# Optimization experiments

Hardware: AMD Instinct MI355X
Metric: run time of the kernel (lower is better)

## Reference

```python
import itertools
import jax, jax.numpy as jnp
import numpy as np

# ---- static config (mirrors args) ----
BS = 4; NUM_SEM = 24; C = 4 + NUM_SEM
H_SCREEN = 240; W_SCREEN = 320
FOV = 60.0
RES = 5; Z_RES = 5
MAP_SIZE_CM = 4800 // 2            # global_downscaling = 2
MAP_CELLS = MAP_SIZE_CM // RES     # 480
VR = 100                           # vision_range
AGENT_HEIGHT = 1.55 * 100.0        # cm
MAX_H = int(360 / Z_RES)           # 72
MIN_H = int(-40 / Z_RES)           # -8
MAP_PRED_THR = 1.0; EXP_PRED_THR = 1.0; CAT_PRED_THR = 5.0
SHIFT_X = VR * RES // 2            # 250 cm (shift_loc)
XC = (W_SCREEN - 1.0) / 2.0
ZC = (H_SCREEN - 1.0) / 2.0
FOCAL = (W_SCREEN / 2.0) / float(np.tan(np.deg2rad(FOV / 2.0)))
DEG2RAD = float(np.pi / 180.0)
R2D = 57.29577951308232


def splat_feat_nd(init_grid, feat, coords):
    # init_grid [B,F,D0,D1,D2], feat [B,F,N], coords [B,3,N] in [-1,1]
    B, Fc = init_grid.shape[0], init_grid.shape[1]
    dims = init_grid.shape[2:]
    grid_flat = init_grid.reshape(B, Fc, -1)
    pos_all, wts_all = [], []
    for d in range(len(dims)):
        Dd = dims[d]
        pos = coords[:, d, :] * (Dd / 2.0) + Dd / 2.0   # [B,N]
        fl = jnp.floor(pos)
        pd, wd = [], []
        for off in (0.0, 1.0):
            p = fl + off
            safe = ((p > 0) & (p < Dd)).astype(pos.dtype)
            wd.append((1.0 - jnp.abs(pos - p)) * safe)
            pd.append(p * safe)
        pos_all.append(pd); wts_all.append(wd)
    bidx = jnp.arange(B)[:, None, None]
    fidx = jnp.arange(Fc)[None, :, None]
    for corner in itertools.product((0, 1), repeat=len(dims)):
        index = jnp.zeros_like(pos_all[0][0])
        wts = jnp.ones_like(pos_all[0][0])
        for d in range(len(dims)):
            index = index * dims[d] + pos_all[d][corner[d]]
            wts = wts * wts_all[d][corner[d]]
        idx = index.astype(jnp.int32)[:, None, :]        # [B,1,N]
        grid_flat = grid_flat.at[bidx, fidx, idx].add(feat * wts[:, None, :])
    return jnp.round(grid_flat).reshape(init_grid.shape)


def affine_grid(theta, H, W):
    # align_corners=True base grid; theta [B,2,3] -> grid [B,H,W,2]
    xs = jnp.linspace(-1.0, 1.0, W)
    ys = jnp.linspace(-1.0, 1.0, H)
    gx, gy = jnp.meshgrid(xs, ys)                        # [H,W]
    base = jnp.stack([gx, gy, jnp.ones_like(gx)], axis=-1)
    return jnp.einsum('hwk,bjk->bhwj', base, theta)


def grid_sample(img, grid):
    # bilinear, zero padding, align_corners=True. img [B,C,H,W], grid [B,Ho,Wo,2]
    B, Cc, H, W = img.shape
    ix = (grid[..., 0] + 1.0) * 0.5 * (W - 1)
    iy = (grid[..., 1] + 1.0) * 0.5 * (H - 1)
    x0 = jnp.floor(ix); y0 = jnp.floor(iy)
    x1 = x0 + 1.0; y1 = y0 + 1.0
    wx1 = ix - x0; wx0 = 1.0 - wx1
    wy1 = iy - y0; wy0 = 1.0 - wy1
    bidx = jnp.arange(B)[:, None, None]
    def gather(xi, yi):
        valid = ((xi >= 0) & (xi <= W - 1) & (yi >= 0) & (yi <= H - 1)).astype(img.dtype)
        xc = jnp.clip(xi, 0, W - 1).astype(jnp.int32)
        yc = jnp.clip(yi, 0, H - 1).astype(jnp.int32)
        v = img[bidx, :, yc, xc]                          # [B,Ho,Wo,C]
        return v * valid[..., None]
    out = (gather(x0, y0) * (wx0 * wy0)[..., None]
           + gather(x1, y0) * (wx1 * wy0)[..., None]
           + gather(x0, y1) * (wx0 * wy1)[..., None]
           + gather(x1, y1) * (wx1 * wy1)[..., None])
    return jnp.transpose(out, (0, 3, 1, 2))


def setup_inputs():
    key = jax.random.key(0)
    k1, k2, k3, k4, k5, k6, k7 = jax.random.split(key, 7)
    rgb = jax.random.uniform(k1, (BS, 3, H_SCREEN, W_SCREEN), jnp.float32)
    depth = jax.random.uniform(k2, (BS, 1, H_SCREEN, W_SCREEN), jnp.float32, 50.0, 500.0)  # cm
    seg = jax.random.uniform(k3, (BS, NUM_SEM, H_SCREEN, W_SCREEN), jnp.float32)
    obs = jnp.concatenate([rgb, depth, seg], axis=1)
    pose_obs = jax.random.uniform(k4, (BS, 3), jnp.float32, -0.1, 0.1)
    maps_last = jax.random.uniform(k5, (BS, C, MAP_CELLS, MAP_CELLS), jnp.float32)
    xy = jax.random.uniform(k6, (BS, 2), jnp.float32, 8.0, 16.0)   # meters, inside map
    th = jax.random.uniform(k7, (BS, 1), jnp.float32, -180.0, 180.0)
    poses_last = jnp.concatenate([xy, th], axis=1)
    view_angles = jnp.zeros((BS,), jnp.float32)
    return {"obs": obs, "pose_obs": pose_obs, "maps_last": maps_last,
            "poses_last": poses_last, "view_angles": view_angles, "holding_state": 0}


def _forward(obs, pose_obs, maps_last, poses_last, view_angles):
    bs, c, h, w = obs.shape
    # holding_state == 0 path: mask_err_below = depth < 0
    depth = jnp.where(obs[:, 3] < 0.0, 1e4, obs[:, 3])
    # point cloud from depth (du_scale == 1)
    x_idx = jnp.arange(w, dtype=depth.dtype)
    z_idx = jnp.arange(h - 1, -1, -1).astype(depth.dtype)
    X = (x_idx[None, None, :] - XC) * depth / FOCAL
    Z = (z_idx[None, :, None] - ZC) * depth / FOCAL
    XYZ = jnp.stack([X, depth, Z], axis=-1)              # [bs,h,w,3]
    # camera elevation rotation about x-axis, then add sensor height
    a = view_angles * DEG2RAD
    ca, sa = jnp.cos(a), jnp.sin(a)
    z0 = jnp.zeros_like(ca); o1 = jnp.ones_like(ca)
    Rx = jnp.stack([o1, z0, z0, z0, ca, -sa, z0, sa, ca], -1).reshape(bs, 3, 3)
    XYZ = jnp.einsum('bij,bhwj->bhwi', Rx, XYZ)
    XYZ = XYZ.at[..., 2].add(AGENT_HEIGHT)
    # transform_pose_t with shift_loc: z-rotation by pi/2-pi/2=0, +x shift
    XYZ = XYZ.at[..., 0].add(float(SHIFT_X))
    # normalize to [-1,1] voxel coords
    xy_n = (XYZ[..., :2] / RES - VR // 2.0) / VR * 2.0
    z_n = (XYZ[..., 2] / Z_RES - (MAX_H + MIN_H) // 2.0) / (MAX_H - MIN_H) * 2.0
    coords = jnp.concatenate([xy_n, z_n[..., None]], axis=-1)
    coords = coords.reshape(bs, h * w, 3).transpose(0, 2, 1)            # [bs,3,N]
    feat = jnp.concatenate([jnp.ones((bs, 1, h * w), obs.dtype),
                            obs[:, 4:].reshape(bs, c - 4, h * w)], axis=1)
    init_grid = jnp.zeros((bs, 1 + NUM_SEM, VR, VR, MAX_H - MIN_H), obs.dtype)
    voxels = splat_feat_nd(init_grid, feat, coords).transpose(0, 1, 3, 2, 4)
    min_z = int(15 / Z_RES - MIN_H)
    max_z = int((AGENT_HEIGHT + 1 + 50) / Z_RES - MIN_H)
    agent_height_proj = voxels[..., min_z:max_z].sum(-1)
    all_height_proj = voxels.sum(-1)
    fp_map_pred = jnp.clip(agent_height_proj[:, 0:1] / MAP_PRED_THR, 0.0, 1.0)
    fp_exp_pred = jnp.clip(all_height_proj[:, 0:1] / EXP_PRED_THR, 0.0, 1.0)
    x1 = MAP_CELLS // 2 - VR // 2; x2 = x1 + VR
    y1 = MAP_CELLS // 2; look = VR - 4; y2 = y1 + look
    agent_view = jnp.zeros((bs, c, MAP_CELLS, MAP_CELLS), obs.dtype)
    agent_view = agent_view.at[:, 0:1, y1:y2, x1:x2].set(fp_map_pred[:, :, :look, :])
    agent_view = agent_view.at[:, 1:2, y1:y2, x1:x2].set(fp_exp_pred[:, :, :look, :])
    agent_view = agent_view.at[:, 4:, y1:y2, x1:x2].set(
        jnp.clip(agent_height_proj[:, 1:] / CAT_PRED_THR, 0.0, 1.0)[:, :, :look, :])
    # pose composition (get_new_pose_batch)
    th0 = poses_last[:, 2] / R2D
    ny = poses_last[:, 1] + pose_obs[:, 0] * jnp.sin(th0) + pose_obs[:, 1] * jnp.cos(th0)
    nx = poses_last[:, 0] + pose_obs[:, 0] * jnp.cos(th0) - pose_obs[:, 1] * jnp.sin(th0)
    no = poses_last[:, 2] + pose_obs[:, 2] * R2D
    no = jnp.fmod(no - 180.0, 360.0) + 180.0
    no = jnp.fmod(no + 180.0, 360.0) - 180.0
    current_poses = jnp.stack([nx, ny, no], axis=1)
    st = jax.lax.stop_gradient(current_poses)            # st_pose is .detach()ed
    half = MAP_CELLS // 2
    sx = -(st[:, 0] * 100.0 / RES - half) / half
    sy = -(st[:, 1] * 100.0 / RES - half) / half
    t = (90.0 - st[:, 2]) * DEG2RAD
    ct, s_t = jnp.cos(t), jnp.sin(t)
    zz = jnp.zeros_like(ct); oo = jnp.ones_like(ct)
    theta_rot = jnp.stack([ct, -s_t, zz, s_t, ct, zz], -1).reshape(bs, 2, 3)
    theta_tr = jnp.stack([oo, zz, sx, zz, oo, sy], -1).reshape(bs, 2, 3)
    rot_grid = affine_grid(theta_rot, MAP_CELLS, MAP_CELLS)
    trans_grid = affine_grid(theta_tr, MAP_CELLS, MAP_CELLS)
    rotated = grid_sample(agent_view, rot_grid)
    translated = grid_sample(rotated, trans_grid)
    map_pred = jnp.maximum(maps_last, translated)        # torch.max over stacked pair
    return fp_map_pred, map_pred, current_poses, current_poses


def reference(obs, pose_obs, maps_last, poses_last, view_angles, holding_state):
    # holding_state == 0 path (no object held); branches for 1/2 are host-side numpy.
    return _forward(obs, pose_obs, maps_last, poses_last, view_angles)
```

## Files before the change

kernel.cpp:

```cpp
#include <hip/hip_runtime.h>
#include <math.h>

#define BS 4
#define CC 28
#define NF 25
#define HS 240
#define WSC 320
#define NPIX (HS*WSC)
#define VR 100
#define ZD 80
#define MC 480
#define NCELL (VR*VR)
#define NREC_MAX ((size_t)BS*NPIX*4)
#define NSTRIP 4096
#define CELL_W 8

__device__ __forceinline__ float clip01(float v){ return fminf(fmaxf(v, 0.f), 1.f); }

struct Geo {
    float wx[2], wy[2], wz[2];
    int   xi[2], yi[2], zi[2];
    bool  sx[2], sy[2];
};

__device__ __forceinline__ Geo compute_geo(const float* __restrict__ obs,
                                           const float* __restrict__ view_angles,
                                           int b, int pix){
    int j = pix % WSC;
    int i = pix / WSC;
    float depth = obs[((size_t)(b*CC + 3))*NPIX + pix];
    if (depth < 0.f) depth = 10000.f;
    const float FOCAL = 277.12812921102035f;
    float X = ((float)j - 159.5f) * depth / FOCAL;
    float Z = ((float)(HS-1-i) - 119.5f) * depth / FOCAL;
    float a = view_angles[b] * 0.017453292519943295f;
    float ca = cosf(a), sa = sinf(a);
    float Y2 = ca*depth - sa*Z;
    float Z2 = sa*depth + ca*Z + 155.f;
    float X2 = X + 250.f;

    float px = ((X2/5.f - 50.f)/100.f*2.f)*50.f + 50.f;
    float py = ((Y2/5.f - 50.f)/100.f*2.f)*50.f + 50.f;
    float pz = ((Z2/5.f - 32.f)/80.f*2.f)*40.f + 40.f;

    Geo g;
    float fx = floorf(px), fy = floorf(py), fz = floorf(pz);
    {
        float p0 = fx, p1 = fx + 1.f;
        g.sx[0] = (p0 > 0.f) && (p0 < 100.f);
        g.sx[1] = (p1 > 0.f) && (p1 < 100.f);
        g.wx[0] = g.sx[0] ? (1.f - fabsf(px - p0)) : 0.f;
        g.wx[1] = g.sx[1] ? (1.f - fabsf(px - p1)) : 0.f;
        g.xi[0] = g.sx[0] ? (int)p0 : 0;
        g.xi[1] = g.sx[1] ? (int)p1 : 0;
    }
    {
        float p0 = fy, p1 = fy + 1.f;
        g.sy[0] = (p0 > 0.f) && (p0 < 100.f);
        g.sy[1] = (p1 > 0.f) && (p1 < 100.f);
        g.wy[0] = g.sy[0] ? (1.f - fabsf(py - p0)) : 0.f;
        g.wy[1] = g.sy[1] ? (1.f - fabsf(py - p1)) : 0.f;
        g.yi[0] = g.sy[0] ? (int)p0 : 0;
        g.yi[1] = g.sy[1] ? (int)p1 : 0;
    }
    {
        float p0 = fz, p1 = fz + 1.f;
        bool s0 = (p0 > 0.f) && (p0 < 80.f);
        bool s1 = (p1 > 0.f) && (p1 < 80.f);
        g.wz[0] = s0 ? (1.f - fabsf(pz - p0)) : 0.f;
        g.wz[1] = s1 ? (1.f - fabsf(pz - p1)) : 0.f;
        g.zi[0] = s0 ? (int)p0 : 0;
        g.zi[1] = s1 ? (int)p1 : 0;
    }
    return g;
}

__global__ void pose_kernel(const float* __restrict__ pose_obs,
                            const float* __restrict__ poses_last,
                            float* __restrict__ out_p1,
                            float* __restrict__ out_p2,
                            float* __restrict__ params){
    int b = threadIdx.x;
    if (b >= BS) return;
    const float R2D = 57.29577951308232f;
    float th0 = poses_last[b*3+2] / R2D;
    float s0 = sinf(th0), c0 = cosf(th0);
    float ny = poses_last[b*3+1] + pose_obs[b*3+0]*s0 + pose_obs[b*3+1]*c0;
    float nx = poses_last[b*3+0] + pose_obs[b*3+0]*c0 - pose_obs[b*3+1]*s0;
    float no = poses_last[b*3+2] + pose_obs[b*3+2]*R2D;
    no = fmodf(no - 180.f, 360.f) + 180.f;
    no = fmodf(no + 180.f, 360.f) - 180.f;
    out_p1[b*3+0] = nx; out_p1[b*3+1] = ny; out_p1[b*3+2] = no;
    out_p2[b*3+0] = nx; out_p2[b*3+1] = ny; out_p2[b*3+2] = no;
    const float half = 240.f;
    float sx = -(nx*100.f/5.f - half)/half;
    float sy = -(ny*100.f/5.f - half)/half;
    float t = (90.f - no) * 0.017453292519943295f;
    params[b*4+0] = cosf(t);
    params[b*4+1] = sinf(t);
    params[b*4+2] = sx;
    params[b*4+3] = sy;
}

__global__ __launch_bounds__(256)
void prep_kernel(const float* __restrict__ obs,
                 const float* __restrict__ view_angles,
                 int* __restrict__ counts,
                 float* __restrict__ feat){
    __shared__ float sf[6400];
    int t   = threadIdx.x;
    int tid = blockIdx.x * 256 + t;
    int b   = tid / NPIX;
    int pix = tid % NPIX;

    Geo g = compute_geo(obs, view_angles, b, pix);
    #pragma unroll
    for (int cy = 0; cy < 2; ++cy)
    #pragma unroll
    for (int cx = 0; cx < 2; ++cx){
        if (g.sx[cx] && g.sy[cy] && (g.wx[cx]*g.wy[cy] != 0.f))
            atomicAdd(&counts[b*NCELL + g.yi[cy]*VR + g.xi[cx]], 1);
    }

    #pragma unroll 6
    for (int f = 0; f < 24; ++f)
        sf[t*25 + f] = obs[((size_t)(b*CC + 4 + f))*NPIX + pix];
    __syncthreads();
    size_t base = ((size_t)b*NPIX + (size_t)(pix - t)) * 24;
    for (int q = t; q < 6144; q += 256)
        feat[base + q] = sf[q + q/24];
}

__global__ void scan_kernel(const int* __restrict__ counts,
                            int* __restrict__ bases,
                            int* __restrict__ cursor,
                            int* __restrict__ cell_start){
    __shared__ int part[1024];
    int t = threadIdx.x;
    const int TOT = BS*NCELL;
    const int CH  = 40;
    int beg = t*CH;
    int s = 0;
    for (int i = 0; i < CH; ++i){
        int idx = beg + i;
        if (idx < TOT) s += counts[idx];
    }
    part[t] = s;
    __syncthreads();
    for (int off = 1; off < 1024; off <<= 1){
        int v = (t >= off) ? part[t-off] : 0;
        __syncthreads();
        part[t] += v;
        __syncthreads();
    }
    int total = part[1023];
    int run = (t == 0) ? 0 : part[t-1];
    for (int i = 0; i < CH; ++i){
        int idx = beg + i;
        if (idx < TOT){
            bases[idx]  = run;
            cursor[idx] = run;
            run += counts[idx];
        }
    }
    __syncthreads();

    int totw  = total + CELL_W*TOT;
    int quota = (totw + NSTRIP - 1) / NSTRIP;
    if (quota < 1) quota = 1;
    for (int i = 0; i < CH; ++i){
        int idx = beg + i;
        if (idx >= TOT) continue;
        int g1 = (bases[idx] + CELL_W*idx) / quota;
        if (g1 > NSTRIP-1) g1 = NSTRIP-1;
        int g0 = -1;
        if (idx > 0){
            g0 = (bases[idx-1] + CELL_W*(idx-1)) / quota;
            if (g0 > NSTRIP-1) g0 = NSTRIP-1;
        }
        for (int gg = g0+1; gg <= g1; ++gg) cell_start[gg] = idx;
        if (idx == TOT-1)
            for (int gg = g1+1; gg <= NSTRIP; ++gg) cell_start[gg] = TOT;
    }
}

__global__ __launch_bounds__(256)
void scatter_kernel(const float* __restrict__ obs,
                    const float* __restrict__ view_angles,
                    int* __restrict__ cursor,
                    uint4* __restrict__ records){
    int tid = blockIdx.x * 256 + threadIdx.x;
    int b   = tid / NPIX;
    int pix = tid % NPIX;
    Geo g = compute_geo(obs, view_angles, b, pix);
    #pragma unroll
    for (int cy = 0; cy < 2; ++cy)
    #pragma unroll
    for (int cx = 0; cx < 2; ++cx){
        float wxy = g.wx[cx] * g.wy[cy];
        if (g.sx[cx] && g.sy[cy] && (wxy != 0.f)){
            int cid = b*NCELL + g.yi[cy]*VR + g.xi[cx];
            int pos = atomicAdd(&cursor[cid], 1);
            float w0 = wxy * g.wz[0];
            float w1 = wxy * g.wz[1];
            unsigned iw = (unsigned)pix | ((unsigned)g.zi[0] << 17)
                                        | ((unsigned)g.zi[1] << 24);
            records[pos] = make_uint4(__float_as_uint(w0), __float_as_uint(w1), iw, 0u);
        }
    }
}

__global__ __launch_bounds__(64)
void accum_kernel(const uint4* __restrict__ records,
                  const float* __restrict__ feat,
                  const int* __restrict__ bases,
                  const int* __restrict__ cursor,
                  const int* __restrict__ cell_start,
                  float* __restrict__ ahp,
                  float* __restrict__ allp,
                  float* __restrict__ out0){
    __shared__ float col[ZD*NF];
    __shared__ uint4 srec[64];

    int g  = blockIdx.x;
    int t  = threadIdx.x;
    int f  = t & 31;
    int rr = t >> 5;
    bool flane = (f < NF);

    int c0 = cell_start[g];
    int c1 = cell_start[g+1];

    for (int cid = c0; cid < c1; ++cid){
        int b    = cid / NCELL;
        int rest = cid - b*NCELL;
        int y = rest / VR;
        int x = rest - y*VR;
        int start = bases[cid];
        int end   = cursor[cid];

        if (start >= end){
            if (t < NF)
                ahp[(((size_t)b*NF + t)*VR + y)*VR + x] = 0.f;
            if (t == 0){
                allp[((size_t)b*VR + y)*VR + x] = 0.f;
                out0[(size_t)b*NCELL + y*VR + x] = 0.f;
            }
            continue;
        }

        const float* feat_b = feat + (size_t)b*NPIX*24;

        float4* col4 = (float4*)col;
        #pragma unroll
        for (int i = 0; i < 8; ++i){
            int idx = t + i*64;
            if (idx < 500) col4[idx] = make_float4(0.f,0.f,0.f,0.f);
        }

        int n0 = end - start; if (n0 > 64) n0 = 64;
        uint4 cur = (t < n0) ? records[start + t] : make_uint4(0u,0u,0u,0u);

        for (int cb = start; cb < end; cb += 64){
            int n = end - cb; if (n > 64) n = 64;
            srec[t] = cur;
            int nb = cb + 64;
            if (nb < end){
                int n2 = end - nb; if (n2 > 64) n2 = 64;
                cur = (t < n2) ? records[nb + t] : make_uint4(0u,0u,0u,0u);
            }
            for (int sub = 0; sub < n; sub += 8){
                uint4 R[4]; float V[4]; bool valid[4];
                #pragma unroll
                for (int u = 0; u < 4; ++u){
                    int idx = sub + 2*u + rr;
                    valid[u] = flane && (idx < n);
                    R[u] = valid[u] ? srec[idx] : make_uint4(0u,0u,0u,0u);
                }
                #pragma unroll
                for (int u = 0; u < 4; ++u){
                    V[u] = 1.f;
                    if (valid[u] && f != 0){
                        int pix = (int)(R[u].z & 0x1FFFFu);
                        V[u] = feat_b[(size_t)pix*24 + (f-1)];
                    }
                }
                #pragma unroll
                for (int u = 0; u < 4; ++u){
                    if (valid[u]){
                        float w0 = __uint_as_float(R[u].x);
                        float w1 = __uint_as_float(R[u].y);
                        unsigned iw = R[u].z;
                        int z0 = (int)((iw >> 17) & 0x7Fu);
                        int z1 = (int)((iw >> 24) & 0x7Fu);
                        if (w0 != 0.f) atomicAdd(&col[z0*NF + f], V[u]*w0);
                        if (w1 != 0.f) atomicAdd(&col[z1*NF + f], V[u]*w1);
                    }
                }
            }
        }

        int f2 = (t < 50) ? (t % NF) : 0;
        int q  = (t < 50) ? (t / NF) : 0;
        float sall = 0.f, sag = 0.f;
        for (int z = q*40; z < q*40 + 40; ++z){
            float rv = rintf(col[z*NF + f2]);
            sall += rv;
            if (z >= 11 && z < 49) sag += rv;
        }
        float sall_o = __shfl(sall, (t + 25) & 63, 64);
        float sag_o  = __shfl(sag,  (t + 25) & 63, 64);
        if (t < NF){
            float a = sag  + sag_o;
            float s = sall + sall_o;
            ahp[(((size_t)b*NF + t)*VR + y)*VR + x] = a;
            if (t == 0){
                allp[((size_t)b*VR + y)*VR + x] = s;
                out0[(size_t)b*NCELL + y*VR + x] = clip01(a);
            }
        }
    }
}

__global__ __launch_bounds__(256)
void final_kernel(const float* __restrict__ ahp,
                  const float* __restrict__ allp,
                  const float* __restrict__ params,
                  const float* __restrict__ maps_last,
                  float* __restrict__ out1){
    int tid = blockIdx.x * blockDim.x + threadIdx.x;
    if (tid >= BS*MC*MC) return;
    int w = tid % MC;
    int h = (tid / MC) % MC;
    int b = tid / (MC*MC);

    float ct = params[b*4+0], st = params[b*4+1];
    float sx = params[b*4+2], sy = params[b*4+3];

    float gx = -1.f + 2.f*(float)w/479.f;
    float gy = -1.f + 2.f*(float)h/479.f;
    float ix = (gx + sx + 1.f)*0.5f*479.f;
    float iy = (gy + sy + 1.f)*0.5f*479.f;
    float x0 = floorf(ix), y0 = floorf(iy);
    float wx1 = ix - x0, wx0 = 1.f - wx1;
    float wy1 = iy - y0, wy0 = 1.f - wy1;

    int   offs[16];
    float wt16[16];
    int nz = 0;
    #pragma unroll
    for (int tc = 0; tc < 4; ++tc){
        float txf = (tc & 1) ? x0 + 1.f : x0;
        float tyf = (tc & 2) ? y0 + 1.f : y0;
        float wt  = ((tc & 1) ? wx1 : wx0) * ((tc & 2) ? wy1 : wy0);
        bool validT = (txf >= 0.f) && (txf <= 479.f) && (tyf >= 0.f) && (tyf <= 479.f);
        int txc = (int)fminf(fmaxf(txf, 0.f), 479.f);
        int tyc = (int)fminf(fmaxf(tyf, 0.f), 479.f);

        float gx2 = -1.f + 2.f*(float)txc/479.f;
        float gy2 = -1.f + 2.f*(float)tyc/479.f;
        float rgx = ct*gx2 - st*gy2;
        float rgy = st*gx2 + ct*gy2;
        float ixr = (rgx + 1.f)*0.5f*479.f;
        float iyr = (rgy + 1.f)*0.5f*479.f;
        float rx0 = floorf(ixr), ry0 = floorf(iyr);
        float rwx1 = ixr - rx0, rwx0 = 1.f - rwx1;
        float rwy1 = iyr - ry0, rwy0 = 1.f - rwy1;

        #pragma unroll
        for (int rc = 0; rc < 4; ++rc){
            int id = tc*4 + rc;
            float rxf = (rc & 1) ? rx0 + 1.f : rx0;
            float ryf = (rc & 2) ? ry0 + 1.f : ry0;
            float wr  = ((rc & 1) ? rwx1 : rwx0) * ((rc & 2) ? rwy1 : rwy0);
            bool validR = (rxf >= 0.f) && (rxf <= 479.f) && (ryf >= 0.f) && (ryf <= 479.f);
            int rxc = (int)fminf(fmaxf(rxf, 0.f), 479.f);
            int ryc = (int)fminf(fmaxf(ryf, 0.f), 479.f);
            bool inwin = validT && validR &&
                         (rxc >= 190) && (rxc < 290) && (ryc >= 240) && (ryc < 336);
            float wgt = wt * wr;
            if (inwin && wgt != 0.f){
                offs[id] = (ryc - 240)*VR + (rxc - 190);
                wt16[id] = wgt;
                nz++;
            } else {
                offs[id] = -1;
                wt16[id] = 0.f;
            }
        }
    }

    size_t outBase = (size_t)b*CC*MC*MC + (size_t)h*MC + w;
    if (nz == 0){
        #pragma unroll
        for (int ch = 0; ch < CC; ++ch){
            size_t o = outBase + (size_t)ch*MC*MC;
            out1[o] = fmaxf(maps_last[o], 0.f);
        }
        return;
    }

    const float* ahp_b  = ahp  + (size_t)b*NF*VR*VR;
    const float* allp_b = allp + (size_t)b*VR*VR;
    for (int ch = 0; ch < CC; ++ch){
        float acc = 0.f;
        if (ch != 2 && ch != 3){
            #pragma unroll
            for (int id = 0; id < 16; ++id){
                if (offs[id] >= 0){
                    float v;
                    if (ch == 0)      v = clip01(ahp_b[offs[id]]);
                    else if (ch == 1) v = clip01(allp_b[offs[id]]);
                    else              v = clip01(ahp_b[(size_t)(ch-3)*VR*VR + offs[id]] / 5.f);
                    acc += wt16[id] * v;
                }
            }
        }
        size_t o = outBase + (size_t)ch*MC*MC;
        out1[o] = fmaxf(maps_last[o], acc);
    }
}

extern "C" void kernel_launch(void* const* d_in, const int* in_sizes, int n_in,
                              void* d_out, int out_size, void* d_ws, size_t ws_size,
                              hipStream_t stream){
    const float* obs         = (const float*)d_in[0];
    const float* pose_obs    = (const float*)d_in[1];
    const float* maps_last   = (const float*)d_in[2];
    const float* poses_last  = (const float*)d_in[3];
    const float* view_angles = (const float*)d_in[4];
    float* out = (float*)d_out;

    const size_t OUT0 = (size_t)BS*VR*VR;
    const size_t OUT1 = (size_t)BS*CC*MC*MC;
    float* out0 = out;
    float* out1 = out + OUT0;
    float* out2 = out + OUT0 + OUT1;
    float* out3 = out2 + BS*3;

    const size_t AHP_FLOATS  = (size_t)BS*NF*VR*VR;
    const size_t ALLP_FLOATS = (size_t)BS*VR*VR;
    const size_t NCID        = (size_t)BS*NCELL;
    const size_t FEAT_FLOATS = (size_t)BS*NPIX*24;
    const size_t CS_INTS     = NSTRIP + 1;

    float* ahp    = (float*)d_ws;
    float* allp   = ahp  + AHP_FLOATS;
    float* params = allp + ALLP_FLOATS;
    char*  ws_tail = (char*)(params + 16);
    size_t ws_used_small = (size_t)(ws_tail - (char*)d_ws);

    const size_t BIG_BYTES = NCID*3*4 + CS_INTS*4 + 64 + NREC_MAX*16 + FEAT_FLOATS*4;
    char* big;
    if (ws_size >= ws_used_small + BIG_BYTES){
        big = ws_tail;
    } else {
        big = (char*)(out1 + OUT1) - BIG_BYTES;
        big = (char*)((uintptr_t)big & ~(uintptr_t)15);
    }
    int* counts     = (int*)big;
    int* bases      = counts + NCID;
    int* cursor     = bases  + NCID;
    int* cell_start = cursor + NCID;
    uint4* records = (uint4*)(((uintptr_t)(cell_start + CS_INTS) + 15) & ~(uintptr_t)15);
    float* feat    = (float*)(records + NREC_MAX);

    hipMemsetAsync(counts, 0, NCID*4, stream);
    pose_kernel<<<1, 64, 0, stream>>>(pose_obs, poses_last, out2, out3, params);

    int nblk = (BS*NPIX)/256;
    prep_kernel<<<nblk, 256, 0, stream>>>(obs, view_angles, counts, feat);
    scan_kernel<<<1, 1024, 0, stream>>>(counts, bases, cursor, cell_start);
    scatter_kernel<<<nblk, 256, 0, stream>>>(obs, view_angles, cursor, records);
    accum_kernel<<<NSTRIP, 64, 0, stream>>>(records, feat, bases, cursor, cell_start,
                                            ahp, allp, out0);
    final_kernel<<<(BS*MC*MC + 255)/256, 256, 0, stream>>>(ahp, allp, params,
                                                           maps_last, out1);
}
```

Before: 1.015 ms.

## Interleave per-cell channel rows and double-buffer gathers in accumulation kernel

Per-cell outputs (25 feature channels plus the all-height sum) move from channel-planar arrays into a contiguous 28-float row per cell. The final kernel can then read each of its 16 bilinear taps with float4 loads and accumulate all channels in registers. The scan now balances strips by a per-cell cost estimate (records plus fixed overhead) and doubles the strip count. The accumulation kernel preloads cell bases into shared memory, prefetches the next cell's records, and double-buffers feature gathers 16 records at a time. The larger register arrays risk lower occupancy and spills.

```diff
diff --git a/kernel.cpp b/kernel.cpp
--- a/kernel.cpp
+++ b/kernel.cpp
@@ -12,8 +12,8 @@
 #define MC 480
 #define NCELL (VR*VR)
 #define NREC_MAX ((size_t)BS*NPIX*4)
-#define NSTRIP 4096
-#define CELL_W 8
+#define NSTRIP 8192
+#define ROWS 28
 
 __device__ __forceinline__ float clip01(float v){ return fminf(fmaxf(v, 0.f), 1.f); }
 
@@ -135,52 +135,47 @@
                             int* __restrict__ bases,
                             int* __restrict__ cursor,
                             int* __restrict__ cell_start){
-    __shared__ int part[1024];
+    __shared__ int partC[1024], partW[1024];
     int t = threadIdx.x;
     const int TOT = BS*NCELL;
     const int CH  = 40;
     int beg = t*CH;
-    int s = 0;
+    int sc = 0, sw = 0;
     for (int i = 0; i < CH; ++i){
         int idx = beg + i;
-        if (idx < TOT) s += counts[idx];
-    }
-    part[t] = s;
+        if (idx < TOT){ int c = counts[idx]; sc += c; sw += c + (c ? 24 : 6); }
+    }
+    partC[t] = sc; partW[t] = sw;
     __syncthreads();
     for (int off = 1; off < 1024; off <<= 1){
-        int v = (t >= off) ? part[t-off] : 0;
+        int vc = (t >= off) ? partC[t-off] : 0;
+        int vw = (t >= off) ? partW[t-off] : 0;
         __syncthreads();
-        part[t] += v;
+        partC[t] += vc; partW[t] += vw;
         __syncthreads();
     }
-    int total = part[1023];
-    int run = (t == 0) ? 0 : part[t-1];
+    int totw  = partW[1023];
+    int quota = (totw + NSTRIP - 1) / NSTRIP;
+    if (quota < 1) quota = 1;
+    int runC = (t == 0) ? 0 : partC[t-1];
+    int runW = (t == 0) ? 0 : partW[t-1];
+    if (t == 0) cell_start[0] = 0;
     for (int i = 0; i < CH; ++i){
         int idx = beg + i;
-        if (idx < TOT){
-            bases[idx]  = run;
-            cursor[idx] = run;
-            run += counts[idx];
-        }
-    }
-    __syncthreads();
-
-    int totw  = total + CELL_W*TOT;
-    int quota = (totw + NSTRIP - 1) / NSTRIP;
-    if (quota < 1) quota = 1;
-    for (int i = 0; i < CH; ++i){
-        int idx = beg + i;
-        if (idx >= TOT) continue;
-        int g1 = (bases[idx] + CELL_W*idx) / quota;
-        if (g1 > NSTRIP-1) g1 = NSTRIP-1;
-        int g0 = -1;
-        if (idx > 0){
-            g0 = (bases[idx-1] + CELL_W*(idx-1)) / quota;
-            if (g0 > NSTRIP-1) g0 = NSTRIP-1;
-        }
-        for (int gg = g0+1; gg <= g1; ++gg) cell_start[gg] = idx;
-        if (idx == TOT-1)
-            for (int gg = g1+1; gg <= NSTRIP; ++gg) cell_start[gg] = TOT;
+        if (idx >= TOT) break;
+        int c = counts[idx];
+        bases[idx]  = runC;
+        cursor[idx] = runC;
+        int w = c + (c ? 24 : 6);
+        int sCur = runW / quota; if (sCur > NSTRIP-1) sCur = NSTRIP-1;
+        runC += c; runW += w;
+        int sNext = runW / quota; if (sNext > NSTRIP-1) sNext = NSTRIP-1;
+        if (idx == TOT-1){
+            bases[TOT] = runC;
+            for (int gg = sCur+1; gg <= NSTRIP; ++gg) cell_start[gg] = TOT;
+        } else {
+            for (int gg = sCur+1; gg <= sNext; ++gg) cell_start[gg] = idx+1;
+        }
     }
 }
 
@@ -210,121 +205,147 @@
     }
 }
 
-__global__ __launch_bounds__(64)
+#define GATHER(S, SUB) do{ \
+  _Pragma("unroll") \
+  for (int u = 0; u < 8; ++u){ \
+    int idx = (SUB) + 2*u + rr; \
+    bool ok = flane && (idx < n); \
+    uint4 rcv = ok ? srec[idx] : Zq; \
+    w##S##0[u] = __uint_as_float(rcv.x); \
+    w##S##1[u] = __uint_as_float(rcv.y); \
+    iw##S[u] = rcv.z; \
+    v##S[u] = 1.f; } \
+  _Pragma("unroll") \
+  for (int u = 0; u < 8; ++u){ \
+    int idx = (SUB) + 2*u + rr; \
+    if (flane && (idx < n) && f != 0){ \
+      int pixq = (int)(iw##S[u] & 0x1FFFFu); \
+      v##S[u] = feat_b[(size_t)pixq*24 + (f-1)]; } } \
+}while(0)
+
+#define FLUSH(S, SUB) do{ \
+  _Pragma("unroll") \
+  for (int u = 0; u < 8; ++u){ \
+    int idx = (SUB) + 2*u + rr; \
+    if (flane && (idx < n)){ \
+      unsigned iwv = iw##S[u]; \
+      int z0 = (int)((iwv >> 17) & 0x7Fu); \
+      int z1 = (int)((iwv >> 24) & 0x7Fu); \
+      float w0 = w##S##0[u], w1 = w##S##1[u]; \
+      if (w0 != 0.f) atomicAdd(&col[z0*NF + f], v##S[u]*w0); \
+      if (w1 != 0.f) atomicAdd(&col[z1*NF + f], v##S[u]*w1); } } \
+}while(0)
+
+__global__ __launch_bounds__(64, 4)
 void accum_kernel(const uint4* __restrict__ records,
                   const float* __restrict__ feat,
                   const int* __restrict__ bases,
-                  const int* __restrict__ cursor,
                   const int* __restrict__ cell_start,
                   float* __restrict__ ahp,
-                  float* __restrict__ allp,
                   float* __restrict__ out0){
     __shared__ float col[ZD*NF];
     __shared__ uint4 srec[64];
-
-    int g  = blockIdx.x;
-    int t  = threadIdx.x;
+    __shared__ int   sb[132];
+
+    int g = blockIdx.x;
+    int t = threadIdx.x;
+    int c0 = cell_start[g];
+    int c1 = cell_start[g+1];
+    int nc = c1 - c0;
+    if (nc <= 0) return;
     int f  = t & 31;
     int rr = t >> 5;
     bool flane = (f < NF);
 
-    int c0 = cell_start[g];
-    int c1 = cell_start[g+1];
-
-    for (int cid = c0; cid < c1; ++cid){
-        int b    = cid / NCELL;
-        int rest = cid - b*NCELL;
-        int y = rest / VR;
-        int x = rest - y*VR;
-        int start = bases[cid];
-        int end   = cursor[cid];
-
+    for (int i = t; i <= nc; i += 64) sb[i] = bases[c0 + i];
+    {   float4* c4 = (float4*)col;
+        #pragma unroll
+        for (int i = 0; i < 8; ++i){ int idx = t + i*64; if (idx < 500) c4[idx] = make_float4(0,0,0,0); } }
+
+    const uint4 Zq = make_uint4(0u,0u,0u,0u);
+    uint4 cur = Zq;
+    bool pf = false;
+
+    for (int ci = 0; ci < nc; ++ci){
+        int start = sb[ci], end = sb[ci+1];
+        int cid = c0 + ci;
         if (start >= end){
-            if (t < NF)
-                ahp[(((size_t)b*NF + t)*VR + y)*VR + x] = 0.f;
-            if (t == 0){
-                allp[((size_t)b*VR + y)*VR + x] = 0.f;
-                out0[(size_t)b*NCELL + y*VR + x] = 0.f;
-            }
+            float* row = ahp + (size_t)cid*ROWS;
+            if (t < ROWS) row[t] = 0.f;
+            if (t == 0)  out0[cid] = 0.f;
             continue;
         }
-
+        int b = cid / NCELL;
         const float* feat_b = feat + (size_t)b*NPIX*24;
 
-        float4* col4 = (float4*)col;
-        #pragma unroll
-        for (int i = 0; i < 8; ++i){
-            int idx = t + i*64;
-            if (idx < 500) col4[idx] = make_float4(0.f,0.f,0.f,0.f);
-        }
-
-        int n0 = end - start; if (n0 > 64) n0 = 64;
-        uint4 cur = (t < n0) ? records[start + t] : make_uint4(0u,0u,0u,0u);
+        if (!pf){
+            int n0 = end - start; if (n0 > 64) n0 = 64;
+            cur = (t < n0) ? records[start + t] : Zq;
+        }
+        pf = false;
 
         for (int cb = start; cb < end; cb += 64){
             int n = end - cb; if (n > 64) n = 64;
             srec[t] = cur;
-            int nb = cb + 64;
-            if (nb < end){
-                int n2 = end - nb; if (n2 > 64) n2 = 64;
-                cur = (t < n2) ? records[nb + t] : make_uint4(0u,0u,0u,0u);
-            }
-            for (int sub = 0; sub < n; sub += 8){
-                uint4 R[4]; float V[4]; bool valid[4];
-                #pragma unroll
-                for (int u = 0; u < 4; ++u){
-                    int idx = sub + 2*u + rr;
-                    valid[u] = flane && (idx < n);
-                    R[u] = valid[u] ? srec[idx] : make_uint4(0u,0u,0u,0u);
-                }
-                #pragma unroll
-                for (int u = 0; u < 4; ++u){
-                    V[u] = 1.f;
-                    if (valid[u] && f != 0){
-                        int pix = (int)(R[u].z & 0x1FFFFu);
-                        V[u] = feat_b[(size_t)pix*24 + (f-1)];
-                    }
-                }
-                #pragma unroll
-                for (int u = 0; u < 4; ++u){
-                    if (valid[u]){
-                        float w0 = __uint_as_float(R[u].x);
-                        float w1 = __uint_as_float(R[u].y);
-                        unsigned iw = R[u].z;
-                        int z0 = (int)((iw >> 17) & 0x7Fu);
-                        int z1 = (int)((iw >> 24) & 0x7Fu);
-                        if (w0 != 0.f) atomicAdd(&col[z0*NF + f], V[u]*w0);
-                        if (w1 != 0.f) atomicAdd(&col[z1*NF + f], V[u]*w1);
-                    }
+            if (cb + 64 < end){
+                int n2 = end - cb - 64; if (n2 > 64) n2 = 64;
+                cur = (t < n2) ? records[cb + 64 + t] : Zq;
+            } else if (ci + 1 < nc){
+                int s2 = sb[ci+1], e2 = sb[ci+2];
+                if (s2 < e2){
+                    int n2 = e2 - s2; if (n2 > 64) n2 = 64;
+                    cur = (t < n2) ? records[s2 + t] : Zq;
+                    pf = true;
                 }
             }
-        }
-
-        int f2 = (t < 50) ? (t % NF) : 0;
-        int q  = (t < 50) ? (t / NF) : 0;
-        float sall = 0.f, sag = 0.f;
-        for (int z = q*40; z < q*40 + 40; ++z){
-            float rv = rintf(col[z*NF + f2]);
-            sall += rv;
-            if (z >= 11 && z < 49) sag += rv;
-        }
-        float sall_o = __shfl(sall, (t + 25) & 63, 64);
-        float sag_o  = __shfl(sag,  (t + 25) & 63, 64);
-        if (t < NF){
-            float a = sag  + sag_o;
-            float s = sall + sall_o;
-            ahp[(((size_t)b*NF + t)*VR + y)*VR + x] = a;
-            if (t == 0){
-                allp[((size_t)b*VR + y)*VR + x] = s;
-                out0[(size_t)b*NCELL + y*VR + x] = clip01(a);
+            float wA0[8], wA1[8], vA[8]; unsigned iwA[8];
+            float wB0[8], wB1[8], vB[8]; unsigned iwB[8];
+            GATHER(A, 0);
+            for (int sub = 0; sub < n; ){
+                int nx = sub + 16;
+                if (nx < n) GATHER(B, nx);
+                FLUSH(A, sub);
+                sub = nx; if (sub >= n) break;
+                nx = sub + 16;
+                if (nx < n) GATHER(A, nx);
+                FLUSH(B, sub);
+                sub = nx;
             }
         }
+
+        {
+            int f2 = t % NF, q = t / NF;
+            float sall = 0.f, sag = 0.f;
+            if (t < 50){
+                for (int z = q*40; z < q*40 + 40; ++z){
+                    float rv = rintf(col[z*NF + f2]);
+                    sall += rv;
+                    if (z >= 11 && z < 49) sag += rv;
+                }
+            }
+            float sall_o = __shfl(sall, (t + 25) & 63, 64);
+            float sag_o  = __shfl(sag,  (t + 25) & 63, 64);
+            float* row = ahp + (size_t)cid*ROWS;
+            if (t < NF){
+                float a = sag + sag_o;
+                float s = sall + sall_o;
+                row[t] = a;
+                if (t == 0){
+                    row[25] = s;
+                    out0[cid] = clip01(a);
+                }
+            } else if (t == 26 || t == 27){
+                row[t] = 0.f;
+            }
+        }
+        {   float4* c4 = (float4*)col;
+            #pragma unroll
+            for (int i = 0; i < 8; ++i){ int idx = t + i*64; if (idx < 500) c4[idx] = make_float4(0,0,0,0); } }
     }
 }
 
 __global__ __launch_bounds__(256)
 void final_kernel(const float* __restrict__ ahp,
-                  const float* __restrict__ allp,
                   const float* __restrict__ params,
                   const float* __restrict__ maps_last,
                   float* __restrict__ out1){
@@ -400,24 +421,41 @@
         return;
     }
 
-    const float* ahp_b  = ahp  + (size_t)b*NF*VR*VR;
-    const float* allp_b = allp + (size_t)b*VR*VR;
+    const float* ahp_b = ahp + (size_t)b*NCELL*ROWS;
+    float acc[26];
+    #pragma unroll
+    for (int k = 0; k < 26; ++k) acc[k] = 0.f;
+
+    #pragma unroll
+    for (int id = 0; id < 16; ++id){
+        if (offs[id] < 0) continue;
+        float v[28];
+        {
+            const float4* rp = (const float4*)(ahp_b + (size_t)offs[id]*ROWS);
+            #pragma unroll
+            for (int k = 0; k < 7; ++k){
+                float4 r = rp[k];
+                v[4*k]   = r.x; v[4*k+1] = r.y;
+                v[4*k+2] = r.z; v[4*k+3] = r.w;
+            }
+        }
+        float wgt = wt16[id];
+        acc[0] += wgt * clip01(v[0]);
+        acc[1] += wgt * clip01(v[25]);
+        #pragma unroll
+        for (int ff = 1; ff < 25; ++ff)
+            acc[1+ff] += wgt * clip01(v[ff] / 5.f);
+    }
+
+    #pragma unroll
     for (int ch = 0; ch < CC; ++ch){
-        float acc = 0.f;
-        if (ch != 2 && ch != 3){
-            #pragma unroll
-            for (int id = 0; id < 16; ++id){
-                if (offs[id] >= 0){
-                    float v;
-                    if (ch == 0)      v = clip01(ahp_b[offs[id]]);
-                    else if (ch == 1) v = clip01(allp_b[offs[id]]);
-                    else              v = clip01(ahp_b[(size_t)(ch-3)*VR*VR + offs[id]] / 5.f);
-                    acc += wt16[id] * v;
-                }
-            }
-        }
+        float a;
+        if (ch == 0)      a = acc[0];
+        else if (ch == 1) a = acc[1];
+        else if (ch < 4)  a = 0.f;
+        else              a = acc[ch-2];
         size_t o = outBase + (size_t)ch*MC*MC;
-        out1[o] = fmaxf(maps_last[o], acc);
+        out1[o] = fmaxf(maps_last[o], a);
     }
 }
 
@@ -438,19 +476,17 @@
     float* out2 = out + OUT0 + OUT1;
     float* out3 = out2 + BS*3;
 
-    const size_t AHP_FLOATS  = (size_t)BS*NF*VR*VR;
-    const size_t ALLP_FLOATS = (size_t)BS*VR*VR;
+    const size_t AHP_FLOATS  = (size_t)BS*NCELL*ROWS;
     const size_t NCID        = (size_t)BS*NCELL;
     const size_t FEAT_FLOATS = (size_t)BS*NPIX*24;
     const size_t CS_INTS     = NSTRIP + 1;
 
     float* ahp    = (float*)d_ws;
-    float* allp   = ahp  + AHP_FLOATS;
-    float* params = allp + ALLP_FLOATS;
+    float* params = ahp + AHP_FLOATS;
     char*  ws_tail = (char*)(params + 16);
     size_t ws_used_small = (size_t)(ws_tail - (char*)d_ws);
 
-    const size_t BIG_BYTES = NCID*3*4 + CS_INTS*4 + 64 + NREC_MAX*16 + FEAT_FLOATS*4;
+    const size_t BIG_BYTES = (NCID*3 + 1 + CS_INTS)*4 + 64 + NREC_MAX*16 + FEAT_FLOATS*4;
     char* big;
     if (ws_size >= ws_used_small + BIG_BYTES){
         big = ws_tail;
@@ -460,7 +496,7 @@
     }
     int* counts     = (int*)big;
     int* bases      = counts + NCID;
-    int* cursor     = bases  + NCID;
+    int* cursor     = bases + NCID + 1;
     int* cell_start = cursor + NCID;
     uint4* records = (uint4*)(((uintptr_t)(cell_start + CS_INTS) + 15) & ~(uintptr_t)15);
     float* feat    = (float*)(records + NREC_MAX);
@@ -472,8 +508,8 @@
     prep_kernel<<<nblk, 256, 0, stream>>>(obs, view_angles, counts, feat);
     scan_kernel<<<1, 1024, 0, stream>>>(counts, bases, cursor, cell_start);
     scatter_kernel<<<nblk, 256, 0, stream>>>(obs, view_angles, cursor, records);
-    accum_kernel<<<NSTRIP, 64, 0, stream>>>(records, feat, bases, cursor, cell_start,
-                                            ahp, allp, out0);
-    final_kernel<<<(BS*MC*MC + 255)/256, 256, 0, stream>>>(ahp, allp, params,
+    accum_kernel<<<NSTRIP, 64, 0, stream>>>(records, feat, bases, cell_start,
+                                            ahp, out0);
+    final_kernel<<<(BS*MC*MC + 255)/256, 256, 0, stream>>>(ahp, params,
                                                            maps_last, out1);
 }
```

Result: faster. 861.9 us (-15.1%).
